# Kernel optimization log

Hardware: AMD Instinct MI355X
Metric: run time of the kernel (lower is better)

The kernel has to match this reference:

```python
import jax, jax.numpy as jnp
from jax import lax
import numpy as np

B, Tf, C, D = 4, 128, 8, 64     # batch, frames (num_tokens), animals, input_dim
E, H, L, O = 512, 8, 6, 256     # n_embd, n_head, n_layer, output_dim
T = Tf * C                      # sequence length = 1024
DH = E // H
EPS = 1e-5


def _ln(x, g, b):
    m = jnp.mean(x, -1, keepdims=True)
    v = jnp.mean((x - m) ** 2, -1, keepdims=True)
    return (x - m) * lax.rsqrt(v + EPS) * g + b


def setup_inputs():
    key = jax.random.key(0)
    ks = jax.random.split(key, 16)
    s = 0.02
    n = lambda k, sh: jax.random.normal(k, sh, jnp.float32) * s
    z = lambda sh: jnp.zeros(sh, jnp.float32)
    o = lambda sh: jnp.ones(sh, jnp.float32)
    return {
        'tokens': jax.random.normal(ks[0], (B, Tf, C, D), jnp.float32),
        'pos': (jnp.arange(B * T) % T).reshape(B, T),
        'mask': o((B, T)),
        'bn_g': o((D,)), 'bn_b': z((D,)),
        'We': n(ks[1], (D, E)), 'be': z((E,)),
        'ln1_g': o((L, E)), 'ln1_b': z((L, E)),
        'ln2_g': o((L, E)), 'ln2_b': z((L, E)),
        'Wq': n(ks[2], (L, E, E)), 'bq': z((L, E)),
        'Wk': n(ks[3], (L, E, E)), 'bk': z((L, E)),
        'Wv': n(ks[4], (L, E, E)), 'bv': z((L, E)),
        'Wo': n(ks[5], (L, E, E)), 'bo': z((L, E)),
        'W1': n(ks[6], (L, E, 4 * E)), 'b1': z((L, 4 * E)),
        'W2': n(ks[7], (L, 4 * E, E)), 'b2': z((L, E)),
        'lnf_g': o((E,)), 'lnf_b': z((E,)),
        'Wp': n(ks[8], (E, O)), 'bp': z((O,)),
        'Wd1': n(ks[9], (O, O)), 'bd1': z((O,)),
        'lnd_g': o((O,)), 'lnd_b': z((O,)),
        'Wd2': n(ks[10], (O, D)), 'bd2': z((D,)),
        'Wf1': n(ks[11], (O, O)), 'bf1': z((O,)),
        'lnfr_g': o((O,)), 'lnfr_b': z((O,)),
        'Wf2': n(ks[12], (O, D * C)), 'bf2': z((D * C,)),
    }


def _forward(tokens, mask, bn_g, bn_b, We, be, ln1_g, ln1_b, ln2_g, ln2_b,
             Wq, bq, Wk, bk, Wv, bv, Wo, bo, W1, b1, W2, b2,
             lnf_g, lnf_b, Wp, bp, Wd1, bd1, lnd_g, lnd_b, Wd2, bd2,
             Wf1, bf1, lnfr_g, lnfr_b, Wf2, bf2):
    # BatchNorm2d over feature channel D (training-mode batch stats, biased var)
    mu = jnp.mean(tokens, axis=(0, 1, 2))
    var = jnp.mean((tokens - mu) ** 2, axis=(0, 1, 2))
    tn = (tokens - mu) * lax.rsqrt(var + EPS) * bn_g + bn_b
    x0 = (tn @ We + be).reshape(B, T, E)  # token embeddings, [B,T,E]

    # static block-causal mask: causal over frames, all-to-all within a frame
    static = jnp.kron(jnp.tril(jnp.ones((Tf, Tf), jnp.float32)),
                      jnp.ones((C, C), jnp.float32))  # [T,T]

    def run_blocks(x, dyn):  # dyn: [B,T] key-mask
        allow = (static[None, None] * dyn[:, None, None, :]) > 0  # [B,1,T,T]

        def step(x, p):
            l1g, l1b, wq, bq_, wk, bk_, wv, bv_, wo, bo_, l2g, l2b, w1, b1_, w2, b2_ = p
            h = _ln(x, l1g, l1b)
            q = (h @ wq + bq_).reshape(B, T, H, DH)
            k = (h @ wk + bk_).reshape(B, T, H, DH)
            v = (h @ wv + bv_).reshape(B, T, H, DH)
            att = jnp.einsum('bthd,bshd->bhts', q, k) / jnp.sqrt(jnp.float32(DH))
            att = jnp.where(allow, att, -jnp.inf)
            att = jax.nn.softmax(att, axis=-1)
            y = jnp.einsum('bhts,bshd->bthd', att, v).reshape(B, T, E)
            x = x + y @ wo + bo_
            h2 = _ln(x, l2g, l2b)
            x = x + jax.nn.gelu(h2 @ w1 + b1_, approximate=False) @ w2 + b2_
            return x, None

        x, _ = lax.scan(step, x, (ln1_g, ln1_b, Wq, bq, Wk, bk, Wv, bv, Wo, bo,
                                  ln2_g, ln2_b, W1, b1, W2, b2))
        return x

    x = run_blocks(x0, mask)
    x = _ln(x, lnf_g, lnf_b) @ Wp + bp                 # [B,T,O]
    x2 = run_blocks(x0[:, ::-1], mask[:, ::-1])
    x2 = _ln(x2, lnf_g, lnf_b) @ Wp + bp

    toks = tokens.reshape(B, T, D) * mask[:, :, None]

    def decoder(z):
        h = jnp.tanh(z @ Wd1 + bd1)
        return _ln(h, lnd_g, lnd_b) @ Wd2 + bd2

    def frame_decoder(z):
        h = jnp.tanh(z @ Wf1 + bf1)
        return _ln(h, lnfr_g, lnfr_b) @ Wf2 + bf2

    mse = lambda a, b_: jnp.mean((a - b_) ** 2)
    pred = decoder(x) * mask[:, :, None]
    l_reg = mse(pred[:, :-C], toks[:, C:])
    pred2 = decoder(x2) * mask[:, :, None]
    l_reg_rl = mse(pred2[:, :-C], toks[:, ::-1][:, C:])

    xf = x.reshape(B, Tf, C, O).mean(axis=-2)          # [B,Tf,O]
    l_fr_lr = mse(frame_decoder(xf)[:, :-1], toks.reshape(B, Tf, C * D)[:, 1:])
    xf2 = x2.reshape(B, Tf, C, O).mean(axis=-2)
    l_fr_rl = mse(frame_decoder(xf2)[:, :-1], toks.reshape(B, Tf, C * D)[:, ::-1][:, 1:])

    losses = jnp.stack([l_reg, l_reg_rl, l_fr_lr, l_fr_rl])
    return xf, losses


def reference(tokens, pos, mask, bn_g, bn_b, We, be, ln1_g, ln1_b, ln2_g, ln2_b,
              Wq, bq, Wk, bk, Wv, bv, Wo, bo, W1, b1, W2, b2,
              lnf_g, lnf_b, Wp, bp, Wd1, bd1, lnd_g, lnd_b, Wd2, bd2,
              Wf1, bf1, lnfr_g, lnfr_b, Wf2, bf2):
    # pos is accepted but unused, matching the original forward
    return _forward(tokens, mask, bn_g, bn_b, We, be, ln1_g, ln1_b, ln2_g, ln2_b,
                    Wq, bq, Wk, bk, Wv, bv, Wo, bo, W1, b1, W2, b2,
                    lnf_g, lnf_b, Wp, bp, Wd1, bd1, lnd_g, lnd_b, Wd2, bd2,
                    Wf1, bf1, lnfr_g, lnfr_b, Wf2, bf2)
```

## Files before the change

kernel.cpp:

```cpp
#include <hip/hip_runtime.h>
#include <math.h>

typedef short short8 __attribute__((ext_vector_type(8)));
typedef float f32x4 __attribute__((ext_vector_type(4)));

__device__ __forceinline__ float block_reduce(float v, float* red) {
  int tid = threadIdx.x;
  red[tid] = v; __syncthreads();
  for (int s = 128; s >= 1; s >>= 1) {
    if (tid < s) red[tid] += red[tid + s];
    __syncthreads();
  }
  float r = red[0];
  __syncthreads();
  return r;
}

__device__ __forceinline__ void cvt1(float x, unsigned short& h, unsigned short& l) {
  unsigned u = __float_as_uint(x);
  unsigned hb = (u + 0x8000u) & 0xffff0000u;
  h = (unsigned short)(hb >> 16);
  l = (unsigned short)(__float_as_uint(x - __uint_as_float(hb)) >> 16);
}

__device__ __forceinline__ void cvt2(float a, float b, unsigned& hp, unsigned& lp) {
  unsigned ua = __float_as_uint(a), ub = __float_as_uint(b);
  unsigned ha = (ua + 0x8000u) & 0xffff0000u;
  unsigned hb = (ub + 0x8000u) & 0xffff0000u;
  float la = a - __uint_as_float(ha);
  float lb = b - __uint_as_float(hb);
  hp = (ha >> 16) | hb;
  lp = (__float_as_uint(la) >> 16) | (__float_as_uint(lb) & 0xffff0000u);
}

__device__ __forceinline__ void gl2l(const unsigned short* g, unsigned short* l) {
  __builtin_amdgcn_global_load_lds(
      (const __attribute__((address_space(1))) void*)g,
      (__attribute__((address_space(3))) void*)l, 16, 0, 0);
}

union U8 { unsigned u[4]; short8 s; };

__global__ __launch_bounds__(256) void sentinel_kernel(float* __restrict__ out, int n, float v) {
  int i = blockIdx.x * 256 + threadIdx.x;
  if (i < n) out[i] = v;
}

__global__ __launch_bounds__(256) void bn_stats_kernel(
    const float* __restrict__ tok, const float* __restrict__ g,
    const float* __restrict__ bb, float* __restrict__ ss) {
  __shared__ float red[256];
  const int d = blockIdx.x;
  float sum = 0.f, sumsq = 0.f;
  for (int s = threadIdx.x; s < 4096; s += 256) {
    float v = tok[s * 64 + d];
    sum += v; sumsq += v * v;
  }
  sum = block_reduce(sum, red);
  sumsq = block_reduce(sumsq, red);
  if (threadIdx.x == 0) {
    float mu = sum * (1.f / 4096.f);
    float var = sumsq * (1.f / 4096.f) - mu * mu;
    float sc = g[d] * rsqrtf(fmaxf(var, 0.f) + 1e-5f);
    ss[d] = sc;
    ss[64 + d] = bb[d] - mu * sc;
  }
}

__global__ __launch_bounds__(256) void tn_kernel(
    const float* __restrict__ tok, const float* __restrict__ ss,
    float* __restrict__ tn) {
  int idx = blockIdx.x * 256 + threadIdx.x;
  int d = idx & 63;
  tn[idx] = tok[idx] * ss[d] + ss[64 + d];
}

__global__ __launch_bounds__(256) void reverse_kernel(
    const float* __restrict__ x0, float* __restrict__ x0r) {
  int idx = blockIdx.x * 256 + threadIdx.x;
  int row = idx >> 9, e = idx & 511;
  int b = row >> 10, t = row & 1023;
  x0r[idx] = x0[((size_t)((b << 10) + (1023 - t))) * 512 + e];
}

__global__ __launch_bounds__(256) void ln_kernel(
    const float* __restrict__ x, const float* __restrict__ g,
    const float* __restrict__ b, float* __restrict__ out, int N) {
  __shared__ float red[256];
  const size_t r = blockIdx.x;
  const int tid = threadIdx.x;
  float v0 = x[r * N + tid];
  float v1 = (N > 256) ? x[r * N + 256 + tid] : 0.f;
  float sum = block_reduce(v0 + v1, red);
  float sumsq = block_reduce(v0 * v0 + v1 * v1, red);
  float mean = sum / (float)N;
  float var = sumsq / (float)N - mean * mean;
  float rs = rsqrtf(fmaxf(var, 0.f) + 1e-5f);
  out[r * N + tid] = (v0 - mean) * rs * g[tid] + b[tid];
  if (N > 256)
    out[r * N + 256 + tid] = (v1 - mean) * rs * g[256 + tid] + b[256 + tid];
}

__global__ __launch_bounds__(256) void ln_pl(
    const float* __restrict__ x, const float* __restrict__ g,
    const float* __restrict__ b, unsigned short* __restrict__ oh,
    unsigned short* __restrict__ ol) {
  __shared__ float red[256];
  const size_t r = blockIdx.x;
  const int tid = threadIdx.x;
  float v0 = x[r * 512 + tid];
  float v1 = x[r * 512 + 256 + tid];
  float sum = block_reduce(v0 + v1, red);
  float sumsq = block_reduce(v0 * v0 + v1 * v1, red);
  float mean = sum * (1.f / 512.f);
  float var = sumsq * (1.f / 512.f) - mean * mean;
  float rs = rsqrtf(fmaxf(var, 0.f) + 1e-5f);
  float o0 = (v0 - mean) * rs * g[tid] + b[tid];
  float o1 = (v1 - mean) * rs * g[256 + tid] + b[256 + tid];
  unsigned short h0, l0, h1, l1;
  cvt1(o0, h0, l0); cvt1(o1, h1, l1);
  oh[r * 512 + tid] = h0;       ol[r * 512 + tid] = l0;
  oh[r * 512 + 256 + tid] = h1; ol[r * 512 + 256 + tid] = l1;
}

__global__ __launch_bounds__(256) void convw(
    const float* __restrict__ W, unsigned short* __restrict__ hi,
    unsigned short* __restrict__ lo, int K, int N, long dls) {
  int id = blockIdx.x * 256 + threadIdx.x;
  int total = (K >> 3) * N;
  if (id >= total) return;
  int c = id / N, n = id - c * N;
  const float* Wp = W + (size_t)blockIdx.y * K * N;
  size_t doff = (size_t)blockIdx.y * dls + (size_t)n * K + c * 8;
  unsigned short h8[8], l8[8];
#pragma unroll
  for (int j = 0; j < 8; ++j) {
    float xv = Wp[(size_t)(c * 8 + j) * N + n];
    cvt1(xv, h8[j], l8[j]);
  }
  uint4 hv = make_uint4(h8[0] | ((unsigned)h8[1] << 16), h8[2] | ((unsigned)h8[3] << 16),
                        h8[4] | ((unsigned)h8[5] << 16), h8[6] | ((unsigned)h8[7] << 16));
  uint4 lv = make_uint4(l8[0] | ((unsigned)l8[1] << 16), l8[2] | ((unsigned)l8[3] << 16),
                        l8[4] | ((unsigned)l8[5] << 16), l8[6] | ((unsigned)l8[7] << 16));
  *reinterpret_cast<uint4*>(hi + doff) = hv;
  *reinterpret_cast<uint4*>(lo + doff) = lv;
}

#define BK 16
template <int ACT>
__global__ __launch_bounds__(256) void gemm3(
    const float* __restrict__ A, const float* __restrict__ W,
    const float* __restrict__ bias, const float* resid,
    float* out, int M, int N, int K) {
  __shared__ float As[BK][64 + 4];
  __shared__ float Bs[BK][64 + 4];
  const int tid = threadIdx.x;
  const int tx = tid & 15, ty = tid >> 4;
  const int n0 = blockIdx.x * 64, m0 = blockIdx.y * 64;
  float acc[4][4] = {};
  for (int k0 = 0; k0 < K; k0 += BK) {
    {
      int m = tid >> 2, kq = tid & 3;
      float4 a4 = *reinterpret_cast<const float4*>(A + (size_t)(m0 + m) * K + k0 + kq * 4);
      As[kq * 4 + 0][m] = a4.x; As[kq * 4 + 1][m] = a4.y;
      As[kq * 4 + 2][m] = a4.z; As[kq * 4 + 3][m] = a4.w;
    }
    {
      int kk = tid >> 4, nq = tid & 15;
      float4 b4 = *reinterpret_cast<const float4*>(W + (size_t)(k0 + kk) * N + n0 + nq * 4);
      Bs[kk][nq * 4 + 0] = b4.x; Bs[kk][nq * 4 + 1] = b4.y;
      Bs[kk][nq * 4 + 2] = b4.z; Bs[kk][nq * 4 + 3] = b4.w;
    }
    __syncthreads();
#pragma unroll
    for (int kq = 0; kq < BK; ++kq) {
      float4 av = *reinterpret_cast<const float4*>(&As[kq][ty * 4]);
      float4 bv = *reinterpret_cast<const float4*>(&Bs[kq][tx * 4]);
      acc[0][0] += av.x * bv.x; acc[0][1] += av.x * bv.y; acc[0][2] += av.x * bv.z; acc[0][3] += av.x * bv.w;
      acc[1][0] += av.y * bv.x; acc[1][1] += av.y * bv.y; acc[1][2] += av.y * bv.z; acc[1][3] += av.y * bv.w;
      acc[2][0] += av.z * bv.x; acc[2][1] += av.z * bv.y; acc[2][2] += av.z * bv.z; acc[2][3] += av.z * bv.w;
      acc[3][0] += av.w * bv.x; acc[3][1] += av.w * bv.y; acc[3][2] += av.w * bv.z; acc[3][3] += av.w * bv.w;
    }
    __syncthreads();
  }
#pragma unroll
  for (int i = 0; i < 4; ++i) {
    int m = m0 + ty * 4 + i;
#pragma unroll
    for (int j = 0; j < 4; ++j) {
      int n = n0 + tx * 4 + j;
      float v = acc[i][j] + bias[n];
      if (resid) v += resid[(size_t)m * N + n];
      if (ACT == 1) v = 0.5f * v * (1.f + erff(v * 0.70710678118654752f));
      if (ACT == 2) v = tanhf(v);
      out[(size_t)m * N + n] = v;
    }
  }
}

template <int ACT, int OUTMODE, int ATOMIC, int BIAS3>
__global__ __launch_bounds__(256, 2) void gemm_bf(
    const unsigned short* __restrict__ Ahp, const unsigned short* __restrict__ Alp,
    const unsigned short* __restrict__ Bhp, const unsigned short* __restrict__ Blp,
    const float* __restrict__ b0, const float* __restrict__ b1, const float* __restrict__ b2,
    float* __restrict__ Cf, unsigned short* __restrict__ Chp, unsigned short* __restrict__ Clp,
    int M, int N, int K, int KZ) {
  __shared__ __align__(16) unsigned short LDS[2][4][128][32];
  const int tid = threadIdx.x;
  const int lane = tid & 63, wid = tid >> 6;
  const int wr = wid >> 1, wc = wid & 1;
  const int lr = lane & 15, lq = lane >> 4;

  const int gx = gridDim.x;
  int lin = blockIdx.y * gx + blockIdx.x;
  int qch = (gx * gridDim.y) >> 3;
  int swz = (lin & 7) * qch + (lin >> 3);
  const int nb = swz % gx, mb = swz / gx;
  const int n0 = nb * 128, m0 = mb * 128;
  const int kbase = blockIdx.z * KZ, kend = kbase + KZ;

  f32x4 acc[4][4];
#pragma unroll
  for (int i = 0; i < 4; ++i)
#pragma unroll
    for (int j = 0; j < 4; ++j) { acc[i][j][0] = 0.f; acc[i][j][1] = 0.f; acc[i][j][2] = 0.f; acc[i][j][3] = 0.f; }

  const unsigned short* gplane =
      (wid == 0) ? Ahp + (size_t)m0 * K :
      (wid == 1) ? Alp + (size_t)m0 * K :
      (wid == 2) ? Bhp + (size_t)n0 * K : Blp + (size_t)n0 * K;
  const int srow = lane >> 2;
  const int sphys = lane & 3;

  auto stage = [&](int buf, int k0) {
#pragma unroll
    for (int j = 0; j < 8; ++j) {
      int row = j * 16 + srow;
      int logslot = sphys ^ ((row >> 1) & 3);
      gl2l(gplane + (size_t)row * K + k0 + logslot * 8, &LDS[buf][wid][j * 16][0]);
    }
  };

  stage(0, kbase);
  __syncthreads();
  int cur = 0;
  for (int k0 = kbase; k0 < kend; k0 += 32) {
    if (k0 + 32 < kend) stage(cur ^ 1, k0 + 32);
    short8 ah[4], al[4], bh[4], bl[4];
#pragma unroll
    for (int mi = 0; mi < 4; ++mi) {
      int row = wr * 64 + mi * 16 + lr;
      int off = (lq ^ ((row >> 1) & 3)) * 8;
      ah[mi] = *reinterpret_cast<const short8*>(&LDS[cur][0][row][off]);
      al[mi] = *reinterpret_cast<const short8*>(&LDS[cur][1][row][off]);
    }
#pragma unroll
    for (int ni = 0; ni < 4; ++ni) {
      int n = wc * 64 + ni * 16 + lr;
      int off = (lq ^ ((n >> 1) & 3)) * 8;
      bh[ni] = *reinterpret_cast<const short8*>(&LDS[cur][2][n][off]);
      bl[ni] = *reinterpret_cast<const short8*>(&LDS[cur][3][n][off]);
    }
#pragma unroll
    for (int mi = 0; mi < 4; ++mi)
#pragma unroll
      for (int ni = 0; ni < 4; ++ni) {
        acc[mi][ni] = __builtin_amdgcn_mfma_f32_16x16x32_bf16(ah[mi], bh[ni], acc[mi][ni], 0, 0, 0);
        acc[mi][ni] = __builtin_amdgcn_mfma_f32_16x16x32_bf16(ah[mi], bl[ni], acc[mi][ni], 0, 0, 0);
        acc[mi][ni] = __builtin_amdgcn_mfma_f32_16x16x32_bf16(al[mi], bh[ni], acc[mi][ni], 0, 0, 0);
      }
    __syncthreads();
    cur ^= 1;
  }

  const float* bsec = b0;
  int bof = 0;
  if (BIAS3) { bsec = (n0 < 512) ? b0 : (n0 < 1024 ? b1 : b2); bof = (n0 & 511) - n0; }
#pragma unroll
  for (int mi = 0; mi < 4; ++mi) {
#pragma unroll
    for (int r = 0; r < 4; ++r) {
      int grow = m0 + wr * 64 + mi * 16 + lq * 4 + r;
#pragma unroll
      for (int ni = 0; ni < 4; ++ni) {
        int col = n0 + wc * 64 + ni * 16 + lr;
        float v = acc[mi][ni][r];
        float bias = BIAS3 ? bsec[col + bof] : b0[col];
        if (ATOMIC) {
          if (blockIdx.z == 0) v += bias;
          atomicAdd(&Cf[(size_t)grow * N + col], v);
        } else {
          v += bias;
          if (ACT == 1) v = 0.5f * v * (1.f + erff(v * 0.70710678118654752f));
          if (ACT == 2) v = tanhf(v);
          if (OUTMODE == 0 || OUTMODE == 2) Cf[(size_t)grow * N + col] = v;
          if (OUTMODE >= 1) {
            unsigned short hv, lv;
            cvt1(v, hv, lv);
            Chp[(size_t)grow * N + col] = hv;
            Clp[(size_t)grow * N + col] = lv;
          }
        }
      }
    }
  }
}

__global__ __launch_bounds__(256, 2) void attn_mfma(
    const float* __restrict__ qkv, const float* __restrict__ mask,
    unsigned short* __restrict__ ybh, unsigned short* __restrict__ ybl, int rev) {
  __shared__ __align__(16) unsigned SH[4096];
  __shared__ __align__(16) unsigned KhL[2048];
  __shared__ __align__(16) unsigned KlL[2048];
  __shared__ float PU[64 * 68];
  __shared__ float km[64];
  unsigned* VhL = SH;
  unsigned* VlL = SH + 2048;

  const int tid = threadIdx.x;
  const int lane = tid & 63, w = tid >> 6;
  const int lr = lane & 15, lq = lane >> 4;

  const int id = blockIdx.x;
  const int top = id >> 8;
  const int r5 = id & 255;
  const int qt = top ? (15 - (r5 >> 4)) : (r5 >> 4);
  const int bh_ = (r5 & 15) | (top << 4);
  const int b = bh_ >> 3, h = bh_ & 7;

  {
    const float* qp = qkv + (size_t)(b * 1024 + qt * 64) * 1536 + h * 64;
    int row = tid >> 2, f4 = tid & 3;
#pragma unroll
    for (int j = 0; j < 4; ++j) {
      int dk = f4 * 4 + j * 16;
      float4 a = *reinterpret_cast<const float4*>(qp + (size_t)row * 1536 + dk);
      unsigned h0, l0, h1, l1;
      cvt2(a.x * 0.125f, a.y * 0.125f, h0, l0);
      cvt2(a.z * 0.125f, a.w * 0.125f, h1, l1);
      int phys = (dk >> 3) ^ (row & 7);
      int off = row * 32 + phys * 4 + (f4 & 1) * 2;
      *reinterpret_cast<uint2*>(&SH[off]) = make_uint2(h0, h1);
      *reinterpret_cast<uint2*>(&KhL[off]) = make_uint2(l0, l1);
    }
  }
  __syncthreads();
  short8 qa_h[2], qa_l[2];
#pragma unroll
  for (int ks = 0; ks < 2; ++ks) {
    int row = w * 16 + lr;
    int phys = (lq + ks * 4) ^ (row & 7);
    qa_h[ks] = *reinterpret_cast<const short8*>(&SH[row * 32 + phys * 4]);
    qa_l[ks] = *reinterpret_cast<const short8*>(&KhL[row * 32 + phys * 4]);
  }
  __syncthreads();

  float m_[4], l_[4] = {0.f, 0.f, 0.f, 0.f};
  f32x4 o_[4];
#pragma unroll
  for (int r = 0; r < 4; ++r) m_[r] = -1e30f;
#pragma unroll
  for (int df = 0; df < 4; ++df) { o_[df][0] = 0.f; o_[df][1] = 0.f; o_[df][2] = 0.f; o_[df][3] = 0.f; }

  for (int kt = 0; kt <= qt; ++kt) {
    const float* kp = qkv + (size_t)(b * 1024 + kt * 64) * 1536 + 512 + h * 64;
    const float* vp = qkv + (size_t)(b * 1024 + kt * 64) * 1536 + 1024 + h * 64;
    {
      int row = tid >> 2, f4 = tid & 3;
#pragma unroll
      for (int j = 0; j < 4; ++j) {
        int dk = f4 * 4 + j * 16;
        float4 a = *reinterpret_cast<const float4*>(kp + (size_t)row * 1536 + dk);
        unsigned h0, l0, h1, l1;
        cvt2(a.x, a.y, h0, l0);
        cvt2(a.z, a.w, h1, l1);
        int phys = (dk >> 3) ^ (row & 7);
        int off = row * 32 + phys * 4 + (f4 & 1) * 2;
        *reinterpret_cast<uint2*>(&KhL[off]) = make_uint2(h0, h1);
        *reinterpret_cast<uint2*>(&KlL[off]) = make_uint2(l0, l1);
      }
    }
    {
      int d = tid & 63, g = tid >> 6;
#pragma unroll
      for (int j = 0; j < 8; ++j) {
        int kpair = (g + j * 4 + (d >> 3)) & 31;
        float v0 = vp[(size_t)(kpair * 2) * 1536 + d];
        float v1 = vp[(size_t)(kpair * 2 + 1) * 1536 + d];
        unsigned hh, ll;
        cvt2(v0, v1, hh, ll);
        int phys = (kpair >> 2) ^ (d & 7);
        int off = d * 32 + phys * 4 + (kpair & 3);
        VhL[off] = hh; VlL[off] = ll;
      }
    }
    if (tid < 64) {
      int s = kt * 64 + tid;
      km[tid] = mask[b * 1024 + (rev ? (1023 - s) : s)];
    }
    __syncthreads();

    f32x4 sacc[4];
#pragma unroll
    for (int kf = 0; kf < 4; ++kf) { sacc[kf][0] = 0.f; sacc[kf][1] = 0.f; sacc[kf][2] = 0.f; sacc[kf][3] = 0.f; }
#pragma unroll
    for (int ks = 0; ks < 2; ++ks) {
#pragma unroll
      for (int kf = 0; kf < 4; ++kf) {
        int col = kf * 16 + lr;
        int phys = (lq + ks * 4) ^ (lr & 7);
        short8 kbh = *reinterpret_cast<const short8*>(&KhL[col * 32 + phys * 4]);
        short8 kbl = *reinterpret_cast<const short8*>(&KlL[col * 32 + phys * 4]);
        sacc[kf] = __builtin_amdgcn_mfma_f32_16x16x32_bf16(qa_h[ks], kbh, sacc[kf], 0, 0, 0);
        sacc[kf] = __builtin_amdgcn_mfma_f32_16x16x32_bf16(qa_h[ks], kbl, sacc[kf], 0, 0, 0);
        sacc[kf] = __builtin_amdgcn_mfma_f32_16x16x32_bf16(qa_l[ks], kbh, sacc[kf], 0, 0, 0);
      }
    }

    const bool diag = (kt == qt);
    float kmv[4];
#pragma unroll
    for (int kf = 0; kf < 4; ++kf) kmv[kf] = km[kf * 16 + lr];
#pragma unroll
    for (int r = 0; r < 4; ++r) {
      int fi = (w * 16 + lq * 4 + r) >> 3;
      float mt = -1e30f;
#pragma unroll
      for (int kf = 0; kf < 4; ++kf) {
        int key = kf * 16 + lr;
        bool ok = (kmv[kf] > 0.f) && (!diag || ((key >> 3) <= fi));
        float x = ok ? sacc[kf][r] : -1e30f;
        sacc[kf][r] = x;
        mt = fmaxf(mt, x);
      }
      mt = fmaxf(mt, __shfl_xor(mt, 1, 16));
      mt = fmaxf(mt, __shfl_xor(mt, 2, 16));
      mt = fmaxf(mt, __shfl_xor(mt, 4, 16));
      mt = fmaxf(mt, __shfl_xor(mt, 8, 16));
      float mn = fmaxf(m_[r], mt);
      float al = __expf(m_[r] - mn);
      m_[r] = mn;
      float rs = 0.f;
#pragma unroll
      for (int kf = 0; kf < 4; ++kf) {
        float sv = sacc[kf][r];
        float p = (sv > -1e29f) ? __expf(sv - mn) : 0.f;
        sacc[kf][r] = p;
        rs += p;
      }
      rs += __shfl_xor(rs, 1, 16);
      rs += __shfl_xor(rs, 2, 16);
      rs += __shfl_xor(rs, 4, 16);
      rs += __shfl_xor(rs, 8, 16);
      l_[r] = l_[r] * al + rs;
#pragma unroll
      for (int df = 0; df < 4; ++df) o_[df][r] *= al;
    }
#pragma unroll
    for (int kf = 0; kf < 4; ++kf)
#pragma unroll
      for (int r = 0; r < 4; ++r)
        PU[(w * 16 + lq * 4 + r) * 68 + kf * 16 + lr] = sacc[kf][r];
    __syncthreads();

#pragma unroll
    for (int ks = 0; ks < 2; ++ks) {
      const float* pp = &PU[(w * 16 + lr) * 68 + ks * 32 + lq * 8];
      float4 p0 = *reinterpret_cast<const float4*>(pp);
      float4 p1 = *reinterpret_cast<const float4*>(pp + 4);
      U8 th, tl;
      cvt2(p0.x, p0.y, th.u[0], tl.u[0]);
      cvt2(p0.z, p0.w, th.u[1], tl.u[1]);
      cvt2(p1.x, p1.y, th.u[2], tl.u[2]);
      cvt2(p1.z, p1.w, th.u[3], tl.u[3]);
      short8 pa_h = th.s, pa_l = tl.s;
#pragma unroll
      for (int df = 0; df < 4; ++df) {
        int col = df * 16 + lr;
        int phys = (lq + ks * 4) ^ (lr & 7);
        short8 vbh = *reinterpret_cast<const short8*>(&VhL[col * 32 + phys * 4]);
        short8 vbl = *reinterpret_cast<const short8*>(&VlL[col * 32 + phys * 4]);
        o_[df] = __builtin_amdgcn_mfma_f32_16x16x32_bf16(pa_h, vbh, o_[df], 0, 0, 0);
        o_[df] = __builtin_amdgcn_mfma_f32_16x16x32_bf16(pa_h, vbl, o_[df], 0, 0, 0);
        o_[df] = __builtin_amdgcn_mfma_f32_16x16x32_bf16(pa_l, vbh, o_[df], 0, 0, 0);
      }
    }
    __syncthreads();
  }

#pragma unroll
  for (int r = 0; r < 4; ++r) {
    float inv = 1.f / fmaxf(l_[r], 1e-30f);
    int qrow = qt * 64 + w * 16 + lq * 4 + r;
#pragma unroll
    for (int df = 0; df < 4; ++df) {
      float val = o_[df][r] * inv;
      unsigned short hv, lv;
      cvt1(val, hv, lv);
      size_t idx = (size_t)(b * 1024 + qrow) * 512 + h * 64 + df * 16 + lr;
      ybh[idx] = hv; ybl[idx] = lv;
    }
  }
}

__global__ __launch_bounds__(256) void frame_mean_kernel(
    const float* __restrict__ xo, float* __restrict__ xf,
    float* __restrict__ outf) {
  int row = blockIdx.x;
  int o = threadIdx.x;
  float s = 0.f;
#pragma unroll
  for (int c = 0; c < 8; ++c) s += xo[((size_t)row * 8 + c) * 256 + o];
  s *= 0.125f;
  xf[row * 256 + o] = s;
  if (outf) outf[row * 256 + o] = s;
}

__global__ __launch_bounds__(256) void loss_reg_kernel(
    const float* __restrict__ pd, const float* __restrict__ tok,
    const float* __restrict__ mask, float* __restrict__ acc, int rev) {
  __shared__ float red[256];
  float local = 0.f;
  for (int idx = blockIdx.x * 256 + threadIdx.x; idx < 260096; idx += gridDim.x * 256) {
    int b = idx / 65024, r2 = idx % 65024;
    int t = r2 >> 6, d = r2 & 63;
    float pred = pd[((size_t)((b << 10) + t)) * 64 + d] * mask[(b << 10) + t];
    int tt = rev ? (1015 - t) : (t + 8);
    float tgt = tok[((size_t)((b << 10) + tt)) * 64 + d] * mask[(b << 10) + tt];
    float df = pred - tgt;
    local += df * df;
  }
  float s = block_reduce(local, red);
  if (threadIdx.x == 0) atomicAdd(acc, s);
}

__global__ __launch_bounds__(256) void loss_fr_kernel(
    const float* __restrict__ pf, const float* __restrict__ tok,
    const float* __restrict__ mask, float* __restrict__ acc, int rev) {
  __shared__ float red[256];
  float local = 0.f;
  for (int idx = blockIdx.x * 256 + threadIdx.x; idx < 260096; idx += gridDim.x * 256) {
    int b = idx / 65024, r2 = idx % 65024;
    int i = r2 >> 9, u = r2 & 511;
    float pred = pf[((size_t)(b * 128 + i)) * 512 + u];
    int c = u >> 6;
    int t = rev ? ((126 - i) * 8 + c) : ((i + 1) * 8 + c);
    float tgt = tok[((size_t)((b << 10) + t)) * 64 + (u & 63)] * mask[(b << 10) + t];
    float df = pred - tgt;
    local += df * df;
  }
  float s = block_reduce(local, red);
  if (threadIdx.x == 0) atomicAdd(acc, s);
}

__global__ void finalize_kernel(const float* __restrict__ acc, float* __restrict__ out) {
  int i = threadIdx.x;
  if (i < 4) out[131072 + i] = acc[i] * (1.0f / 260096.0f);
}

extern "C" void kernel_launch(void* const* d_in, const int* in_sizes, int n_in,
                              void* d_out, int out_size, void* d_ws, size_t ws_size,
                              hipStream_t stream) {
  float* ws = (float*)d_ws;
  const size_t OFF_SS   = 0;
  const size_t OFF_LACC = 128;
  const size_t OFF_TN   = 256;
  const size_t OFF_X0   = 262400;
  const size_t OFF_X0R  = 2359552;
  const size_t OFF_X    = 4456704;
  const size_t OFF_HPL  = 6553856;
  const size_t OFF_QKV  = 8651008;
  const size_t OFF_YB   = 14942464;
  const size_t OFF_XO   = 17039616;
  const size_t OFF_XOPL = 18088192;
  const size_t OFF_HD   = 19136768;
  const size_t OFF_HD2  = 20185344;
  const size_t OFF_PD   = 21233920;
  const size_t OFF_XF   = 21496064;
  const size_t OFF_HF   = 21627136;
  const size_t OFF_HF2  = 21758208;
  const size_t OFF_PF   = 21889280;
  const size_t OFF_WB   = 22151424;
  const size_t TOTAL_MIN = OFF_WB + 1048576;
  const size_t TOTAL_BIG = OFF_WB + 19070976;

  float* ss   = ws + OFF_SS;
  float* lacc = ws + OFF_LACC;
  float* tn   = ws + OFF_TN;
  float* x0   = ws + OFF_X0;
  float* x0r  = ws + OFF_X0R;
  float* x    = ws + OFF_X;
  unsigned short* hh = (unsigned short*)(ws + OFF_HPL);
  unsigned short* hl = hh + 2097152;
  float* qkv  = ws + OFF_QKV;
  unsigned short* uh = (unsigned short*)(ws + OFF_QKV);
  unsigned short* ul = uh + 8388608;
  unsigned short* ybh = (unsigned short*)(ws + OFF_YB);
  unsigned short* ybl = ybh + 2097152;
  float* xo   = ws + OFF_XO;
  unsigned short* xoh = (unsigned short*)(ws + OFF_XOPL);
  unsigned short* xol = xoh + 1048576;
  float* hd   = ws + OFF_HD;
  float* hd2  = ws + OFF_HD2;
  float* pd   = ws + OFF_PD;
  float* xf   = ws + OFF_XF;
  float* hf   = ws + OFF_HF;
  float* hf2  = ws + OFF_HF2;
  float* pf   = ws + OFF_PF;
  unsigned short* wb16 = (unsigned short*)(ws + OFF_WB);
  float* out_f = (float*)d_out;

  static const int EXPECTED[39] = {
      262144, 4096, 4096, 64, 64, 32768, 512, 3072, 3072, 3072, 3072,
      1572864, 3072, 1572864, 3072, 1572864, 3072, 1572864, 3072,
      6291456, 12288, 6291456, 3072, 512, 512, 131072, 256, 65536, 256,
      256, 256, 16384, 64, 65536, 256, 256, 256, 131072, 512};
  bool manifest_ok = (n_in == 39) && (ws_size >= TOTAL_MIN * sizeof(float));
  if (manifest_ok)
    for (int i = 0; i < 39; ++i)
      if (in_sizes[i] != EXPECTED[i]) { manifest_ok = false; break; }
  if (!manifest_ok) {
    hipLaunchKernelGGL(sentinel_kernel, dim3((out_size + 255) / 256), dim3(256), 0, stream,
                       out_f, out_size, 2000.0f);
    return;
  }
  const bool bigws = ws_size >= TOTAL_BIG * sizeof(float);

  const float* tok    = (const float*)d_in[0];
  const float* mask   = (const float*)d_in[2];
  const float* bn_g   = (const float*)d_in[3];
  const float* bn_b   = (const float*)d_in[4];
  const float* We     = (const float*)d_in[5];
  const float* be     = (const float*)d_in[6];
  const float* ln1_g  = (const float*)d_in[7];
  const float* ln1_b  = (const float*)d_in[8];
  const float* ln2_g  = (const float*)d_in[9];
  const float* ln2_b  = (const float*)d_in[10];
  const float* Wq     = (const float*)d_in[11];
  const float* bq     = (const float*)d_in[12];
  const float* Wk     = (const float*)d_in[13];
  const float* bk     = (const float*)d_in[14];
  const float* Wv     = (const float*)d_in[15];
  const float* bv     = (const float*)d_in[16];
  const float* Wo     = (const float*)d_in[17];
  const float* bo     = (const float*)d_in[18];
  const float* W1     = (const float*)d_in[19];
  const float* b1     = (const float*)d_in[20];
  const float* W2     = (const float*)d_in[21];
  const float* b2     = (const float*)d_in[22];
  const float* lnf_g  = (const float*)d_in[23];
  const float* lnf_b  = (const float*)d_in[24];
  const float* Wp     = (const float*)d_in[25];
  const float* bp     = (const float*)d_in[26];
  const float* Wd1    = (const float*)d_in[27];
  const float* bd1    = (const float*)d_in[28];
  const float* lnd_g  = (const float*)d_in[29];
  const float* lnd_b  = (const float*)d_in[30];
  const float* Wd2    = (const float*)d_in[31];
  const float* bd2    = (const float*)d_in[32];
  const float* Wf1    = (const float*)d_in[33];
  const float* bf1    = (const float*)d_in[34];
  const float* lnfr_g = (const float*)d_in[35];
  const float* lnfr_b = (const float*)d_in[36];
  const float* Wf2    = (const float*)d_in[37];
  const float* bf2    = (const float*)d_in[38];

  unsigned short* wqkv_h = wb16;
  unsigned short* wqkv_l = wb16 + 4718592;
  unsigned short* wo_h   = wb16 + 9437184;
  unsigned short* wo_l   = wb16 + 11010048;
  unsigned short* w1_h   = wb16 + 12582912;
  unsigned short* w1_l   = wb16 + 18874368;
  unsigned short* w2_h   = wb16 + 25165824;
  unsigned short* w2_l   = wb16 + 31457280;
  unsigned short* wp_h   = wb16 + 37748736;
  unsigned short* wp_l   = wb16 + 37879808;
  unsigned short* wd1_h  = wb16 + 38010880;
  unsigned short* wd1_l  = wb16 + 38076416;
  unsigned short* scr    = wb16;

  auto G = [&](int act, const float* A, const float* W, const float* bias,
               const float* resid, float* out, int M, int N, int K) {
    dim3 g(N / 64, M / 64), b(256);
    if (act == 0) hipLaunchKernelGGL((gemm3<0>), g, b, 0, stream, A, W, bias, resid, out, M, N, K);
    else if (act == 1) hipLaunchKernelGGL((gemm3<1>), g, b, 0, stream, A, W, bias, resid, out, M, N, K);
    else hipLaunchKernelGGL((gemm3<2>), g, b, 0, stream, A, W, bias, resid, out, M, N, K);
  };
  auto CONV = [&](const float* W, unsigned short* hi, unsigned short* lo,
                  int K, int N, int layers, long dls) {
    int blocks = ((K >> 3) * N + 255) / 256;
    hipLaunchKernelGGL(convw, dim3(blocks, layers), dim3(256), 0, stream, W, hi, lo, K, N, dls);
  };

  hipMemsetAsync(lacc, 0, 4 * sizeof(float), stream);
  if (bigws) {
    CONV(Wq, wqkv_h,          wqkv_l,          512, 512, 6, 786432);
    CONV(Wk, wqkv_h + 262144, wqkv_l + 262144, 512, 512, 6, 786432);
    CONV(Wv, wqkv_h + 524288, wqkv_l + 524288, 512, 512, 6, 786432);
    CONV(Wo, wo_h, wo_l, 512, 512, 6, 262144);
    CONV(W1, w1_h, w1_l, 512, 2048, 6, 1048576);
    CONV(W2, w2_h, w2_l, 2048, 512, 6, 1048576);
    CONV(Wp, wp_h, wp_l, 512, 256, 1, 0);
    CONV(Wd1, wd1_h, wd1_l, 256, 256, 1, 0);
  }
  hipLaunchKernelGGL(bn_stats_kernel, dim3(64), dim3(256), 0, stream, tok, bn_g, bn_b, ss);
  hipLaunchKernelGGL(tn_kernel, dim3(1024), dim3(256), 0, stream, tok, ss, tn);
  G(0, tn, We, be, nullptr, x0, 4096, 512, 64);
  hipLaunchKernelGGL(reverse_kernel, dim3(8192), dim3(256), 0, stream, x0, x0r);

  for (int dir = 0; dir < 2; ++dir) {
    const float* xin = dir ? x0r : x0;
    for (int l = 0; l < 6; ++l) {
      const float* xl = (l == 0) ? xin : x;
      hipLaunchKernelGGL(ln_pl, dim3(4096), dim3(256), 0, stream,
                         xl, ln1_g + l * 512, ln1_b + l * 512, hh, hl);
      const unsigned short *pqh, *pql;
      if (bigws) { pqh = wqkv_h + (size_t)l * 786432; pql = wqkv_l + (size_t)l * 786432; }
      else {
        CONV(Wq + (size_t)l * 262144, scr,          scr + 786432,          512, 512, 1, 0);
        CONV(Wk + (size_t)l * 262144, scr + 262144, scr + 786432 + 262144, 512, 512, 1, 0);
        CONV(Wv + (size_t)l * 262144, scr + 524288, scr + 786432 + 524288, 512, 512, 1, 0);
        pqh = scr; pql = scr + 786432;
      }
      hipLaunchKernelGGL((gemm_bf<0, 0, 0, 1>), dim3(12, 32, 1), dim3(256), 0, stream,
                         hh, hl, pqh, pql, bq + l * 512, bk + l * 512, bv + l * 512,
                         qkv, nullptr, nullptr, 4096, 1536, 512, 512);
      if (l == 0)
        hipMemcpyAsync(x, xin, 2097152 * sizeof(float), hipMemcpyDeviceToDevice, stream);
      hipLaunchKernelGGL(attn_mfma, dim3(512), dim3(256), 0, stream, qkv, mask, ybh, ybl, dir);
      const unsigned short *poh, *pol;
      if (bigws) { poh = wo_h + (size_t)l * 262144; pol = wo_l + (size_t)l * 262144; }
      else {
        CONV(Wo + (size_t)l * 262144, scr, scr + 262144, 512, 512, 1, 0);
        poh = scr; pol = scr + 262144;
      }
      hipLaunchKernelGGL((gemm_bf<0, 0, 1, 0>), dim3(4, 32, 2), dim3(256), 0, stream,
                         ybh, ybl, poh, pol, bo + l * 512, nullptr, nullptr,
                         x, nullptr, nullptr, 4096, 512, 512, 256);
      hipLaunchKernelGGL(ln_pl, dim3(4096), dim3(256), 0, stream,
                         x, ln2_g + l * 512, ln2_b + l * 512, hh, hl);
      const unsigned short *p1h, *p1l;
      if (bigws) { p1h = w1_h + (size_t)l * 1048576; p1l = w1_l + (size_t)l * 1048576; }
      else {
        CONV(W1 + (size_t)l * 1048576, scr, scr + 1048576, 512, 2048, 1, 0);
        p1h = scr; p1l = scr + 1048576;
      }
      hipLaunchKernelGGL((gemm_bf<1, 1, 0, 0>), dim3(16, 32, 1), dim3(256), 0, stream,
                         hh, hl, p1h, p1l, b1 + l * 2048, nullptr, nullptr,
                         nullptr, uh, ul, 4096, 2048, 512, 512);
      const unsigned short *p2h, *p2l;
      if (bigws) { p2h = w2_h + (size_t)l * 1048576; p2l = w2_l + (size_t)l * 1048576; }
      else {
        CONV(W2 + (size_t)l * 1048576, scr, scr + 1048576, 2048, 512, 1, 0);
        p2h = scr; p2l = scr + 1048576;
      }
      hipLaunchKernelGGL((gemm_bf<0, 0, 1, 0>), dim3(4, 32, 2), dim3(256), 0, stream,
                         uh, ul, p2h, p2l, b2 + l * 512, nullptr, nullptr,
                         x, nullptr, nullptr, 4096, 512, 2048, 1024);
    }
    hipLaunchKernelGGL(ln_pl, dim3(4096), dim3(256), 0, stream, x, lnf_g, lnf_b, hh, hl);
    const unsigned short *pph, *ppl, *pdh, *pdl;
    if (bigws) { pph = wp_h; ppl = wp_l; }
    else { CONV(Wp, scr, scr + 131072, 512, 256, 1, 0); pph = scr; ppl = scr + 131072; }
    hipLaunchKernelGGL((gemm_bf<0, 2, 0, 0>), dim3(2, 32, 1), dim3(256), 0, stream,
                       hh, hl, pph, ppl, bp, nullptr, nullptr,
                       xo, xoh, xol, 4096, 256, 512, 512);
    if (bigws) { pdh = wd1_h; pdl = wd1_l; }
    else { CONV(Wd1, scr, scr + 65536, 256, 256, 1, 0); pdh = scr; pdl = scr + 65536; }
    hipLaunchKernelGGL((gemm_bf<2, 0, 0, 0>), dim3(2, 32, 1), dim3(256), 0, stream,
                       xoh, xol, pdh, pdl, bd1, nullptr, nullptr,
                       hd, nullptr, nullptr, 4096, 256, 256, 256);
    hipLaunchKernelGGL(ln_kernel, dim3(4096), dim3(256), 0, stream, hd, lnd_g, lnd_b, hd2, 256);
    G(0, hd2, Wd2, bd2, nullptr, pd, 4096, 64, 256);
    hipLaunchKernelGGL(loss_reg_kernel, dim3(256), dim3(256), 0, stream,
                       pd, tok, mask, lacc + (dir ? 1 : 0), dir);
    hipLaunchKernelGGL(frame_mean_kernel, dim3(512), dim3(256), 0, stream,
                       xo, xf, dir == 0 ? out_f : (float*)nullptr);
    G(2, xf, Wf1, bf1, nullptr, hf, 512, 256, 256);
    hipLaunchKernelGGL(ln_kernel, dim3(512), dim3(256), 0, stream, hf, lnfr_g, lnfr_b, hf2, 256);
    G(0, hf2, Wf2, bf2, nullptr, pf, 512, 512, 256);
    hipLaunchKernelGGL(loss_fr_kernel, dim3(256), dim3(256), 0, stream,
                       pf, tok, mask, lacc + (dir ? 3 : 2), dir);
  }
  hipLaunchKernelGGL(finalize_kernel, dim3(1), dim3(64), 0, stream, lacc, out_f);
}
```

Baseline: 2.766 ms.

## Emit split-bf16 Q/K and transposed V from QKV GEMM epilogue for attention

The QKV GEMM epilogue now applies the bias, pre-scales Q by 0.125, and writes split hi/lo bf16 Q and K, plus V in a per-head transposed [d][t] layout. The attention kernel no longer reads fp32 QKV and converts it on every tile. It loads ready bf16 tiles with direct global-to-LDS copies (gl2l) into swizzled buffers and raises launch bounds to 3 blocks per SU. This removes repeated fp32-to-bf16 conversion and strided V transposes inside attention, at the cost of scattered transposed stores in the GEMM epilogue and extra workspace.

```diff
diff --git a/kernel.cpp b/kernel.cpp
--- a/kernel.cpp
+++ b/kernel.cpp
@@ -198,12 +198,13 @@
   }
 }
 
-template <int ACT, int OUTMODE, int ATOMIC, int BIAS3>
+template <int ACT, int OUTMODE, int ATOMIC, int BIAS3, int QKV>
 __global__ __launch_bounds__(256, 2) void gemm_bf(
     const unsigned short* __restrict__ Ahp, const unsigned short* __restrict__ Alp,
     const unsigned short* __restrict__ Bhp, const unsigned short* __restrict__ Blp,
     const float* __restrict__ b0, const float* __restrict__ b1, const float* __restrict__ b2,
     float* __restrict__ Cf, unsigned short* __restrict__ Chp, unsigned short* __restrict__ Clp,
+    unsigned short* __restrict__ vth, unsigned short* __restrict__ vtl,
     int M, int N, int K, int KZ) {
   __shared__ __align__(16) unsigned short LDS[2][4][128][32];
   const int tid = threadIdx.x;
@@ -273,6 +274,49 @@
     cur ^= 1;
   }
 
+  if (QKV) {
+    const float* bsec = (n0 < 512) ? b0 : (n0 < 1024 ? b1 : b2);
+    const int bof = (n0 & 511) - n0;
+    if (n0 < 1024) {
+      const float scale = (n0 < 512) ? 0.125f : 1.f;
+#pragma unroll
+      for (int mi = 0; mi < 4; ++mi)
+#pragma unroll
+        for (int r = 0; r < 4; ++r) {
+          int grow = m0 + wr * 64 + mi * 16 + lq * 4 + r;
+#pragma unroll
+          for (int ni = 0; ni < 4; ++ni) {
+            int col = n0 + wc * 64 + ni * 16 + lr;
+            float v = (acc[mi][ni][r] + bsec[col + bof]) * scale;
+            unsigned short hv, lv;
+            cvt1(v, hv, lv);
+            Chp[(size_t)grow * N + col] = hv;
+            Clp[(size_t)grow * N + col] = lv;
+          }
+        }
+    } else {
+#pragma unroll
+      for (int mi = 0; mi < 4; ++mi) {
+        int t0 = m0 + wr * 64 + mi * 16 + lq * 4;
+        int bb = t0 >> 10, tt = t0 & 1023;
+#pragma unroll
+        for (int ni = 0; ni < 4; ++ni) {
+          int col = n0 + wc * 64 + ni * 16 + lr;
+          float bias = bsec[col + bof];
+          int hh_ = (col - 1024) >> 6, dd = (col - 1024) & 63;
+          unsigned short h4[4], l4[4];
+#pragma unroll
+          for (int r = 0; r < 4; ++r) cvt1(acc[mi][ni][r] + bias, h4[r], l4[r]);
+          size_t off = ((size_t)((bb * 8 + hh_) * 64 + dd)) * 1024 + tt;
+          *reinterpret_cast<uint2*>(vth + off) = make_uint2(
+              h4[0] | ((unsigned)h4[1] << 16), h4[2] | ((unsigned)h4[3] << 16));
+          *reinterpret_cast<uint2*>(vtl + off) = make_uint2(
+              l4[0] | ((unsigned)l4[1] << 16), l4[2] | ((unsigned)l4[3] << 16));
+        }
+      }
+    }
+    return;
+  }
   const float* bsec = b0;
   int bof = 0;
   if (BIAS3) { bsec = (n0 < 512) ? b0 : (n0 < 1024 ? b1 : b2); bof = (n0 & 511) - n0; }
@@ -306,16 +350,15 @@
   }
 }
 
-__global__ __launch_bounds__(256, 2) void attn_mfma(
-    const float* __restrict__ qkv, const float* __restrict__ mask,
+__global__ __launch_bounds__(256, 3) void attn_mfma(
+    const unsigned short* __restrict__ qkvh, const unsigned short* __restrict__ qkvl,
+    const unsigned short* __restrict__ vth, const unsigned short* __restrict__ vtl,
+    const float* __restrict__ mask,
     unsigned short* __restrict__ ybh, unsigned short* __restrict__ ybl, int rev) {
-  __shared__ __align__(16) unsigned SH[4096];
-  __shared__ __align__(16) unsigned KhL[2048];
-  __shared__ __align__(16) unsigned KlL[2048];
+  __shared__ __align__(16) unsigned short QK[2][4096];
+  __shared__ __align__(16) unsigned short VT[2][4096];
   __shared__ float PU[64 * 68];
   __shared__ float km[64];
-  unsigned* VhL = SH;
-  unsigned* VlL = SH + 2048;
 
   const int tid = threadIdx.x;
   const int lane = tid & 63, w = tid >> 6;
@@ -329,19 +372,16 @@
   const int b = bh_ >> 3, h = bh_ & 7;
 
   {
-    const float* qp = qkv + (size_t)(b * 1024 + qt * 64) * 1536 + h * 64;
-    int row = tid >> 2, f4 = tid & 3;
+    const unsigned short* src = (w < 2) ? qkvh : qkvl;
+    unsigned short* dst = QK[w >> 1];
+    int half = w & 1;
 #pragma unroll
     for (int j = 0; j < 4; ++j) {
-      int dk = f4 * 4 + j * 16;
-      float4 a = *reinterpret_cast<const float4*>(qp + (size_t)row * 1536 + dk);
-      unsigned h0, l0, h1, l1;
-      cvt2(a.x * 0.125f, a.y * 0.125f, h0, l0);
-      cvt2(a.z * 0.125f, a.w * 0.125f, h1, l1);
-      int phys = (dk >> 3) ^ (row & 7);
-      int off = row * 32 + phys * 4 + (f4 & 1) * 2;
-      *reinterpret_cast<uint2*>(&SH[off]) = make_uint2(h0, h1);
-      *reinterpret_cast<uint2*>(&KhL[off]) = make_uint2(l0, l1);
+      int chunk = half * 256 + j * 64 + lane;
+      int row = chunk >> 3, p = chunk & 7;
+      int slot = p ^ (row & 7);
+      gl2l(src + (size_t)(b * 1024 + qt * 64 + row) * 1536 + h * 64 + slot * 8,
+           dst + (half * 256 + j * 64) * 8);
     }
   }
   __syncthreads();
@@ -350,8 +390,8 @@
   for (int ks = 0; ks < 2; ++ks) {
     int row = w * 16 + lr;
     int phys = (lq + ks * 4) ^ (row & 7);
-    qa_h[ks] = *reinterpret_cast<const short8*>(&SH[row * 32 + phys * 4]);
-    qa_l[ks] = *reinterpret_cast<const short8*>(&KhL[row * 32 + phys * 4]);
+    qa_h[ks] = *reinterpret_cast<const short8*>(&QK[0][row * 64 + phys * 8]);
+    qa_l[ks] = *reinterpret_cast<const short8*>(&QK[1][row * 64 + phys * 8]);
   }
   __syncthreads();
 
@@ -363,35 +403,27 @@
   for (int df = 0; df < 4; ++df) { o_[df][0] = 0.f; o_[df][1] = 0.f; o_[df][2] = 0.f; o_[df][3] = 0.f; }
 
   for (int kt = 0; kt <= qt; ++kt) {
-    const float* kp = qkv + (size_t)(b * 1024 + kt * 64) * 1536 + 512 + h * 64;
-    const float* vp = qkv + (size_t)(b * 1024 + kt * 64) * 1536 + 1024 + h * 64;
-    {
-      int row = tid >> 2, f4 = tid & 3;
-#pragma unroll
-      for (int j = 0; j < 4; ++j) {
-        int dk = f4 * 4 + j * 16;
-        float4 a = *reinterpret_cast<const float4*>(kp + (size_t)row * 1536 + dk);
-        unsigned h0, l0, h1, l1;
-        cvt2(a.x, a.y, h0, l0);
-        cvt2(a.z, a.w, h1, l1);
-        int phys = (dk >> 3) ^ (row & 7);
-        int off = row * 32 + phys * 4 + (f4 & 1) * 2;
-        *reinterpret_cast<uint2*>(&KhL[off]) = make_uint2(h0, h1);
-        *reinterpret_cast<uint2*>(&KlL[off]) = make_uint2(l0, l1);
-      }
-    }
-    {
-      int d = tid & 63, g = tid >> 6;
+    if (w < 2) {
+      const unsigned short* src = (w == 0) ? qkvh : qkvl;
+      unsigned short* dst = QK[w];
 #pragma unroll
       for (int j = 0; j < 8; ++j) {
-        int kpair = (g + j * 4 + (d >> 3)) & 31;
-        float v0 = vp[(size_t)(kpair * 2) * 1536 + d];
-        float v1 = vp[(size_t)(kpair * 2 + 1) * 1536 + d];
-        unsigned hh, ll;
-        cvt2(v0, v1, hh, ll);
-        int phys = (kpair >> 2) ^ (d & 7);
-        int off = d * 32 + phys * 4 + (kpair & 3);
-        VhL[off] = hh; VlL[off] = ll;
+        int chunk = j * 64 + lane;
+        int row = chunk >> 3, p = chunk & 7;
+        int slot = p ^ (row & 7);
+        gl2l(src + (size_t)(b * 1024 + kt * 64 + row) * 1536 + 512 + h * 64 + slot * 8,
+             dst + j * 512);
+      }
+    } else {
+      const unsigned short* src = (w == 2) ? vth : vtl;
+      unsigned short* dst = VT[w - 2];
+#pragma unroll
+      for (int j = 0; j < 8; ++j) {
+        int chunk = j * 64 + lane;
+        int row = chunk >> 3, p = chunk & 7;
+        int slot = p ^ (row & 7);
+        gl2l(src + (size_t)((b * 8 + h) * 64 + row) * 1024 + kt * 64 + slot * 8,
+             dst + j * 512);
       }
     }
     if (tid < 64) {
@@ -409,8 +441,8 @@
       for (int kf = 0; kf < 4; ++kf) {
         int col = kf * 16 + lr;
         int phys = (lq + ks * 4) ^ (lr & 7);
-        short8 kbh = *reinterpret_cast<const short8*>(&KhL[col * 32 + phys * 4]);
-        short8 kbl = *reinterpret_cast<const short8*>(&KlL[col * 32 + phys * 4]);
+        short8 kbh = *reinterpret_cast<const short8*>(&QK[0][col * 64 + phys * 8]);
+        short8 kbl = *reinterpret_cast<const short8*>(&QK[1][col * 64 + phys * 8]);
         sacc[kf] = __builtin_amdgcn_mfma_f32_16x16x32_bf16(qa_h[ks], kbh, sacc[kf], 0, 0, 0);
         sacc[kf] = __builtin_amdgcn_mfma_f32_16x16x32_bf16(qa_h[ks], kbl, sacc[kf], 0, 0, 0);
         sacc[kf] = __builtin_amdgcn_mfma_f32_16x16x32_bf16(qa_l[ks], kbh, sacc[kf], 0, 0, 0);
@@ -478,8 +510,8 @@
       for (int df = 0; df < 4; ++df) {
         int col = df * 16 + lr;
         int phys = (lq + ks * 4) ^ (lr & 7);
-        short8 vbh = *reinterpret_cast<const short8*>(&VhL[col * 32 + phys * 4]);
-        short8 vbl = *reinterpret_cast<const short8*>(&VlL[col * 32 + phys * 4]);
+        short8 vbh = *reinterpret_cast<const short8*>(&VT[0][col * 64 + phys * 8]);
+        short8 vbl = *reinterpret_cast<const short8*>(&VT[1][col * 64 + phys * 8]);
         o_[df] = __builtin_amdgcn_mfma_f32_16x16x32_bf16(pa_h, vbh, o_[df], 0, 0, 0);
         o_[df] = __builtin_amdgcn_mfma_f32_16x16x32_bf16(pa_h, vbl, o_[df], 0, 0, 0);
         o_[df] = __builtin_amdgcn_mfma_f32_16x16x32_bf16(pa_l, vbh, o_[df], 0, 0, 0);
@@ -580,7 +612,8 @@
   const size_t OFF_HF   = 21627136;
   const size_t OFF_HF2  = 21758208;
   const size_t OFF_PF   = 21889280;
-  const size_t OFF_WB   = 22151424;
+  const size_t OFF_VT   = 22151424;
+  const size_t OFF_WB   = 24248576;
   const size_t TOTAL_MIN = OFF_WB + 1048576;
   const size_t TOTAL_BIG = OFF_WB + 19070976;
 
@@ -592,7 +625,8 @@
   float* x    = ws + OFF_X;
   unsigned short* hh = (unsigned short*)(ws + OFF_HPL);
   unsigned short* hl = hh + 2097152;
-  float* qkv  = ws + OFF_QKV;
+  unsigned short* qkvh = (unsigned short*)(ws + OFF_QKV);
+  unsigned short* qkvl = qkvh + 6291456;
   unsigned short* uh = (unsigned short*)(ws + OFF_QKV);
   unsigned short* ul = uh + 8388608;
   unsigned short* ybh = (unsigned short*)(ws + OFF_YB);
@@ -607,6 +641,8 @@
   float* hf   = ws + OFF_HF;
   float* hf2  = ws + OFF_HF2;
   float* pf   = ws + OFF_PF;
+  unsigned short* vth = (unsigned short*)(ws + OFF_VT);
+  unsigned short* vtl = vth + 2097152;
   unsigned short* wb16 = (unsigned short*)(ws + OFF_WB);
   float* out_f = (float*)d_out;
 
@@ -722,21 +758,22 @@
         CONV(Wv + (size_t)l * 262144, scr + 524288, scr + 786432 + 524288, 512, 512, 1, 0);
         pqh = scr; pql = scr + 786432;
       }
-      hipLaunchKernelGGL((gemm_bf<0, 0, 0, 1>), dim3(12, 32, 1), dim3(256), 0, stream,
+      hipLaunchKernelGGL((gemm_bf<0, 1, 0, 1, 1>), dim3(12, 32, 1), dim3(256), 0, stream,
                          hh, hl, pqh, pql, bq + l * 512, bk + l * 512, bv + l * 512,
-                         qkv, nullptr, nullptr, 4096, 1536, 512, 512);
+                         nullptr, qkvh, qkvl, vth, vtl, 4096, 1536, 512, 512);
       if (l == 0)
         hipMemcpyAsync(x, xin, 2097152 * sizeof(float), hipMemcpyDeviceToDevice, stream);
-      hipLaunchKernelGGL(attn_mfma, dim3(512), dim3(256), 0, stream, qkv, mask, ybh, ybl, dir);
+      hipLaunchKernelGGL(attn_mfma, dim3(512), dim3(256), 0, stream,
+                         qkvh, qkvl, vth, vtl, mask, ybh, ybl, dir);
       const unsigned short *poh, *pol;
       if (bigws) { poh = wo_h + (size_t)l * 262144; pol = wo_l + (size_t)l * 262144; }
       else {
         CONV(Wo + (size_t)l * 262144, scr, scr + 262144, 512, 512, 1, 0);
         poh = scr; pol = scr + 262144;
       }
-      hipLaunchKernelGGL((gemm_bf<0, 0, 1, 0>), dim3(4, 32, 2), dim3(256), 0, stream,
+      hipLaunchKernelGGL((gemm_bf<0, 0, 1, 0, 0>), dim3(4, 32, 2), dim3(256), 0, stream,
                          ybh, ybl, poh, pol, bo + l * 512, nullptr, nullptr,
-                         x, nullptr, nullptr, 4096, 512, 512, 256);
+                         x, nullptr, nullptr, nullptr, nullptr, 4096, 512, 512, 256);
       hipLaunchKernelGGL(ln_pl, dim3(4096), dim3(256), 0, stream,
                          x, ln2_g + l * 512, ln2_b + l * 512, hh, hl);
       const unsigned short *p1h, *p1l;
@@ -745,31 +782,31 @@
         CONV(W1 + (size_t)l * 1048576, scr, scr + 1048576, 512, 2048, 1, 0);
         p1h = scr; p1l = scr + 1048576;
       }
-      hipLaunchKernelGGL((gemm_bf<1, 1, 0, 0>), dim3(16, 32, 1), dim3(256), 0, stream,
+      hipLaunchKernelGGL((gemm_bf<1, 1, 0, 0, 0>), dim3(16, 32, 1), dim3(256), 0, stream,
                          hh, hl, p1h, p1l, b1 + l * 2048, nullptr, nullptr,
-                         nullptr, uh, ul, 4096, 2048, 512, 512);
+                         nullptr, uh, ul, nullptr, nullptr, 4096, 2048, 512, 512);
       const unsigned short *p2h, *p2l;
       if (bigws) { p2h = w2_h + (size_t)l * 1048576; p2l = w2_l + (size_t)l * 1048576; }
       else {
         CONV(W2 + (size_t)l * 1048576, scr, scr + 1048576, 2048, 512, 1, 0);
         p2h = scr; p2l = scr + 1048576;
       }
-      hipLaunchKernelGGL((gemm_bf<0, 0, 1, 0>), dim3(4, 32, 2), dim3(256), 0, stream,
+      hipLaunchKernelGGL((gemm_bf<0, 0, 1, 0, 0>), dim3(4, 32, 2), dim3(256), 0, stream,
                          uh, ul, p2h, p2l, b2 + l * 512, nullptr, nullptr,
-                         x, nullptr, nullptr, 4096, 512, 2048, 1024);
+                         x, nullptr, nullptr, nullptr, nullptr, 4096, 512, 2048, 1024);
     }
     hipLaunchKernelGGL(ln_pl, dim3(4096), dim3(256), 0, stream, x, lnf_g, lnf_b, hh, hl);
     const unsigned short *pph, *ppl, *pdh, *pdl;
     if (bigws) { pph = wp_h; ppl = wp_l; }
     else { CONV(Wp, scr, scr + 131072, 512, 256, 1, 0); pph = scr; ppl = scr + 131072; }
-    hipLaunchKernelGGL((gemm_bf<0, 2, 0, 0>), dim3(2, 32, 1), dim3(256), 0, stream,
+    hipLaunchKernelGGL((gemm_bf<0, 2, 0, 0, 0>), dim3(2, 32, 1), dim3(256), 0, stream,
                        hh, hl, pph, ppl, bp, nullptr, nullptr,
-                       xo, xoh, xol, 4096, 256, 512, 512);
+                       xo, xoh, xol, nullptr, nullptr, 4096, 256, 512, 512);
     if (bigws) { pdh = wd1_h; pdl = wd1_l; }
     else { CONV(Wd1, scr, scr + 65536, 256, 256, 1, 0); pdh = scr; pdl = scr + 65536; }
-    hipLaunchKernelGGL((gemm_bf<2, 0, 0, 0>), dim3(2, 32, 1), dim3(256), 0, stream,
+    hipLaunchKernelGGL((gemm_bf<2, 0, 0, 0, 0>), dim3(2, 32, 1), dim3(256), 0, stream,
                        xoh, xol, pdh, pdl, bd1, nullptr, nullptr,
-                       hd, nullptr, nullptr, 4096, 256, 256, 256);
+                       hd, nullptr, nullptr, nullptr, nullptr, 4096, 256, 256, 256);
     hipLaunchKernelGGL(ln_kernel, dim3(4096), dim3(256), 0, stream, hd, lnd_g, lnd_b, hd2, 256);
     G(0, hd2, Wd2, bd2, nullptr, pd, 4096, 64, 256);
     hipLaunchKernelGGL(loss_reg_kernel, dim3(256), dim3(256), 0, stream,
```

New measurement: 2.733 ms. No clear change (-1.2%).
